# Kernel optimization log

Hardware: AMD Instinct MI355X
Metric: run time of the kernel (lower is better)

## Reference

```python
import jax, jax.numpy as jnp
import numpy as np

N = 100000
LS = (0, 1, 2)
MULS = (128, 64, 32)   # multiplicities of 0e,1o,2e in input1 / mid / out
MUL_Y = 64             # input2 = 64x0e (pure scalars)
DIM_X = sum(m * (2 * l + 1) for m, l in zip(MULS, LS))  # 480


def _split_irreps(x):
    # x: (N, 480) -> list of (N, mul, 2l+1) blocks
    parts, off = [], 0
    for m, l in zip(MULS, LS):
        d = m * (2 * l + 1)
        parts.append(x[:, off:off + d].reshape(-1, m, 2 * l + 1))
        off += d
    return parts


def setup_inputs() -> dict:
    key = jax.random.key(0)
    ks = jax.random.split(key, 8)
    inp = {
        "x": jax.random.normal(ks[0], (N, DIM_X), jnp.float32),
        "y": jax.random.normal(ks[1], (N, MUL_Y), jnp.float32),
    }
    for i, m in enumerate(MULS):
        # e3nn internal weights ~ N(0,1); path normalization applied in forward
        inp[f"W_tp{i}"] = jax.random.normal(ks[2 + i], (m, MUL_Y, m), jnp.float32)
        inp[f"W_lin{i}"] = jax.random.normal(ks[5 + i], (m, m), jnp.float32)
    return inp


def reference(x, y, W_tp0, W_tp1, W_tp2, W_lin0, W_lin1, W_lin2):
    W_tp = (W_tp0, W_tp1, W_tp2)
    W_lin = (W_lin0, W_lin1, W_lin2)
    xs = _split_irreps(x)
    outs = []
    for m, l, Wt, Wl, xl in zip(MULS, LS, W_tp, W_lin, xs):
        # e3nn 'uvw' path with scalar (0e) second input:
        #   CG(l,0,l)[m1,0,mo] = delta / sqrt(2l+1)
        #   path_weight = sqrt(ir_out.dim / (mul1*mul2)) = sqrt((2l+1)/(m*MUL_Y))
        # net coefficient = 1 / sqrt(m * MUL_Y)
        c_tp = float(1.0 / np.sqrt(m * MUL_Y))
        mid = c_tp * jnp.einsum('uvw,num,nv->nwm', Wt, xl, y)  # (N, m, 2l+1)
        # o3.Linear: single path per irrep, weight 1/sqrt(fan_in), fan_in = m
        c_lin = float(1.0 / np.sqrt(m))
        out = c_lin * jnp.einsum('uw,num->nwm', Wl, mid)       # (N, m, 2l+1)
        outs.append(out.reshape(-1, m * (2 * l + 1)))
    return jnp.concatenate(outs, axis=-1)  # (N, 480)
```

## Files before the change

### kernel.cpp

```cpp
#include <hip/hip_runtime.h>


typedef _Float16 f16x8 __attribute__((ext_vector_type(8)));
typedef _Float16 h2    __attribute__((ext_vector_type(2)));
typedef float    f32x4 __attribute__((ext_vector_type(4)));

__device__ __forceinline__ void gload_lds16(const void* g, void* l) {
    __builtin_amdgcn_global_load_lds(
        (const __attribute__((address_space(1))) unsigned*)g,
        (__attribute__((address_space(3))) unsigned*)l, 16, 0, 0);
}

template<int M, int NT>
__global__ void pack_b(const float* __restrict__ Wt, const float* __restrict__ Wl,
                       _Float16* __restrict__ Bp) {
    const int gid = blockIdx.x * 256 + threadIdx.x;
    const int total = M * 64 * M / 2;
    if (gid >= total) return;
    const int w_ = gid & (M - 1);
    const int uvp = gid / M;
    const float4* wtA = (const float4*)(Wt + (size_t)(2 * uvp) * M);
    const float4* wtB = (const float4*)(Wt + (size_t)(2 * uvp + 1) * M);
    float a0 = 0.f, a1 = 0.f;
    #pragma unroll 4
    for (int w = 0; w < M; w += 4) {
        float4 tA = wtA[w >> 2], tB = wtB[w >> 2];
        float l0 = Wl[(w + 0) * M + w_], l1 = Wl[(w + 1) * M + w_];
        float l2 = Wl[(w + 2) * M + w_], l3 = Wl[(w + 3) * M + w_];
        a0 += tA.x * l0 + tA.y * l1 + tA.z * l2 + tA.w * l3;
        a1 += tB.x * l0 + tB.y * l1 + tB.z * l2 + tB.w * l3;
    }
    #pragma unroll
    for (int t = 0; t < 2; ++t) {
        const int uv = 2 * uvp + t;
        const int u = uv >> 6, v = uv & 63;
        const int vh = v >> 5, vv = v & 31, quad = vv >> 3, j = vv & 7;
        const int kc = u * 2 + vh, nt = w_ >> 4, lane = quad * 16 + (w_ & 15);
        Bp[((size_t)(kc * NT + nt) * 64 + lane) * 8 + j] = (_Float16)(t ? a1 : a0);
    }
}

template<int M, int NCOMP, int XOFF, int NT, int KC, int MT>
__device__ __forceinline__ void tp_block(char* smem, int wg,
    const float* __restrict__ x, const float* __restrict__ y,
    const _Float16* __restrict__ Bp, float* __restrict__ out, int Rtot, float cscale)
{
    constexpr int WM = MT / 128;
    constexpr int WN = NT;
    constexpr int UC = KC / 2;
    constexpr int XU = 16;
    constexpr int KTOT = 2 * M;
    constexpr int NCHUNK = KTOT / KC;
    constexpr int CPS = XU / UC;
    constexpr int NSLAB = M / XU;
    constexpr int BCH = KC * NT * 1024;
    constexpr int XSL = MT * XU * 2;
    constexpr int NS_T = MT / NCOMP + 2;
    constexpr int XE = NS_T * XU * NCOMP;
    constexpr int XITER = (XE + 511) / 512;

    char* bb0 = smem;
    char* bb1 = smem + BCH;
    char* xb0 = smem + 2 * BCH;
    char* xb1 = smem + 2 * BCH + XSL;

    const int tid = threadIdx.x;
    const int lane = tid & 63;
    const int wv = tid >> 6;
    const int l15 = lane & 15;
    const int quad = lane >> 4;
    const int r0 = wg * MT;
    const int s0 = r0 / NCOMP;
    const int k0 = r0 - s0 * NCOMP;

    float xt[XITER];
    auto xld = [&](int slab) {
        const int ub = slab * XU;
        #pragma unroll
        for (int i = 0; i < XITER; ++i) {
            const int p = tid + i * 512;
            float v = 0.f;
            if (p < XE) {
                const int sl = p / (XU * NCOMP);
                const int fo = p - sl * (XU * NCOMP);
                const int ul = fo / NCOMP;
                const int k  = fo - ul * NCOMP;
                const int rl = sl * NCOMP + k - k0;
                if (rl >= 0 && rl < MT && (r0 + rl) < Rtot)
                    v = x[(size_t)(s0 + sl) * 480 + XOFF + (ub + ul) * NCOMP + k];
            }
            xt[i] = v;
        }
    };
    auto xwr = [&](char* xd) {
        #pragma unroll
        for (int i = 0; i < XITER; ++i) {
            const int p = tid + i * 512;
            if (p < XE) {
                const int sl = p / (XU * NCOMP);
                const int fo = p - sl * (XU * NCOMP);
                const int ul = fo / NCOMP;
                const int k  = fo - ul * NCOMP;
                const int rl = sl * NCOMP + k - k0;
                if (rl >= 0 && rl < MT)
                    *(_Float16*)(xd + (rl * XU + ul) * 2) = (_Float16)xt[i];
            }
        }
    };
    auto stageB = [&](int c, char* bd) {
        const char* gs = (const char*)Bp + (size_t)c * BCH + wv * 2048 + lane * 16;
        char* ld = bd + wv * 2048;
        gload_lds16(gs, ld);
        gload_lds16(gs + 1024, ld + 1024);
    };

    int rowf[WM];
    union YH { f16x8 v; h2 h[4]; };
    YH yh[2][WM];
    #pragma unroll
    for (int f = 0; f < WM; ++f) {
        rowf[f] = wv * (WM * 16) + f * 16 + l15;
        const int Rg = r0 + rowf[f];
        const int sf = (Rg < Rtot) ? (int)((unsigned)Rg / NCOMP) : 0;
        #pragma unroll
        for (int vh = 0; vh < 2; ++vh) {
            const float4* yp = (const float4*)(y + (size_t)sf * 64 + vh * 32 + quad * 8);
            const float4 a = yp[0], b = yp[1];
            union { f16x8 v; _Float16 e[8]; } t;
            t.e[0] = (_Float16)a.x; t.e[1] = (_Float16)a.y;
            t.e[2] = (_Float16)a.z; t.e[3] = (_Float16)a.w;
            t.e[4] = (_Float16)b.x; t.e[5] = (_Float16)b.y;
            t.e[6] = (_Float16)b.z; t.e[7] = (_Float16)b.w;
            yh[vh][f].v = t.v;
        }
    }

    f32x4 acc[WM][WN];
    #pragma unroll
    for (int f = 0; f < WM; ++f)
        #pragma unroll
        for (int g = 0; g < WN; ++g) acc[f][g] = f32x4{0.f, 0.f, 0.f, 0.f};

    xld(0);
    stageB(0, bb0);
    xwr(xb0);
    __syncthreads();

    int bcur = 0, xcur = 0;
    #pragma unroll 1
    for (int c = 0; c < NCHUNK; ++c) {
        if (c + 1 < NCHUNK) stageB(c + 1, bcur ? bb0 : bb1);
        const int cm = c & (CPS - 1);
        const int sl1 = c / CPS + 1;
        if (cm == 0 && sl1 < NSLAB) xld(sl1);

        const char* bs = bcur ? bb1 : bb0;
        const char* xs = xcur ? xb1 : xb0;
        const int uoff = cm * UC;
        unsigned xv0[WM], xv1[WM];
        #pragma unroll
        for (int f = 0; f < WM; ++f) {
            const char* xa = xs + (rowf[f] * XU + uoff) * 2;
            if constexpr (UC == 1)      xv0[f] = *(const unsigned short*)xa;
            else if constexpr (UC == 2) xv0[f] = *(const unsigned*)xa;
            else { const uint2 t = *(const uint2*)xa; xv0[f] = t.x; xv1[f] = t.y; }
        }
        #pragma unroll
        for (int kl = 0; kl < KC; ++kl) {
            const int vh = kl & 1, uo = kl >> 1;
            f16x8 bg[WN];
            #pragma unroll
            for (int g = 0; g < WN; ++g)
                bg[g] = *(const f16x8*)(bs + (kl * NT + g) * 1024 + lane * 16);
            f16x8 af[WM];
            #pragma unroll
            for (int f = 0; f < WM; ++f) {
                const unsigned d = (UC == 4 && (uo & 2)) ? xv1[f] : xv0[f];
                const unsigned hh = (uo & 1) ? (d >> 16) : (d & 0xffffu);
                union { unsigned u; h2 h; } xb2; xb2.u = hh | (hh << 16);
                union { f16x8 v; h2 h[4]; } a_;
                #pragma unroll
                for (int q = 0; q < 4; ++q) a_.h[q] = xb2.h * yh[vh][f].h[q];
                af[f] = a_.v;
            }
            #pragma unroll
            for (int f = 0; f < WM; ++f)
                #pragma unroll
                for (int g = 0; g < WN; ++g)
                    acc[f][g] = __builtin_amdgcn_mfma_f32_16x16x32_f16(af[f], bg[g], acc[f][g], 0, 0, 0);
        }
        if (cm == CPS - 1 && sl1 < NSLAB) xwr(xcur ? xb0 : xb1);
        __syncthreads();
        bcur ^= 1;
        if (cm == CPS - 1) xcur ^= 1;
    }

    #pragma unroll
    for (int f = 0; f < WM; ++f) {
        #pragma unroll
        for (int g = 0; g < WN; ++g) {
            const int col = g * 16 + l15;
            #pragma unroll
            for (int r = 0; r < 4; ++r) {
                const int R = r0 + wv * (WM * 16) + f * 16 + quad * 4 + r;
                if (R < Rtot) {
                    const int s = (int)((unsigned)R / NCOMP);
                    const int k = R - s * NCOMP;
                    out[(size_t)s * 480 + XOFF + col * NCOMP + k] = acc[f][g][r] * cscale;
                }
            }
        }
    }
}

__global__ __launch_bounds__(512, 2)
void tp_main(const float* __restrict__ x, const float* __restrict__ y,
             const _Float16* __restrict__ B0, const _Float16* __restrict__ B1,
             const _Float16* __restrict__ B2, float* __restrict__ out,
             int R0, int R1, int R2, int G0, int G1)
{
    __shared__ char smem[65536];
    const int b = blockIdx.x;
    if (b < G0)            tp_block<128, 1,   0, 8, 2, 384>(smem, b,           x, y, B0, out, R0, 1.f / 1024.f);
    else if (b < G0 + G1)  tp_block< 64, 3, 128, 4, 4, 512>(smem, b - G0,      x, y, B1, out, R1, 1.f / 512.f);
    else                   tp_block< 32, 5, 320, 2, 8, 512>(smem, b - G0 - G1, x, y, B2, out, R2, 1.f / 256.f);
}

extern "C" void kernel_launch(void* const* d_in, const int* in_sizes, int n_in,
                              void* d_out, int out_size, void* d_ws, size_t ws_size,
                              hipStream_t stream) {
    const float* x   = (const float*)d_in[0];
    const float* y   = (const float*)d_in[1];
    const float* Wt0 = (const float*)d_in[2];
    const float* Wl0 = (const float*)d_in[3];
    const float* Wt1 = (const float*)d_in[4];
    const float* Wl1 = (const float*)d_in[5];
    const float* Wt2 = (const float*)d_in[6];
    const float* Wl2 = (const float*)d_in[7];
    float* out = (float*)d_out;

    const int Ns = in_sizes[0] / 480;

    _Float16* B0 = (_Float16*)d_ws;
    _Float16* B1 = B0 + 8192 * 128;
    _Float16* B2 = B1 + 4096 * 64;

    pack_b<128, 8><<<(128 * 64 * 128 / 2 + 255) / 256, 256, 0, stream>>>(Wt0, Wl0, B0);
    pack_b< 64, 4><<<( 64 * 64 *  64 / 2 + 255) / 256, 256, 0, stream>>>(Wt1, Wl1, B1);
    pack_b< 32, 2><<<( 32 * 64 *  32 / 2 + 255) / 256, 256, 0, stream>>>(Wt2, Wl2, B2);

    const int R0 = Ns, R1 = Ns * 3, R2 = Ns * 5;
    const int G0 = (R0 + 383) / 384;
    const int G1 = (R1 + 511) / 512;
    const int G2 = (R2 + 511) / 512;
    tp_main<<<G0 + G1 + G2, 512, 0, stream>>>(x, y, B0, B1, B2, out, R0, R1, R2, G0, G1);
}
```

Before: 682.1 us.

## Use 4x2 wave tiling and store x as pre-duplicated half2 in padded LDS

Waves are rearranged from an 8x1 split along rows to a 4x2 grid over rows and output columns. Each wave now reads half the B fragments from LDS but builds twice as many A fragments (x times y). The x slab in LDS is now stored as pre-duplicated half2 words with a padded stride of 20, so the inner loop does one vector load and no shift-and-mask to build the broadcast. In exchange, static LDS grows from 64 KiB to 112 KiB. That likely cuts residency from two workgroups per CU to one and weakens latency hiding.

```diff
diff --git a/kernel.cpp b/kernel.cpp
--- a/kernel.cpp
+++ b/kernel.cpp
@@ -45,16 +45,18 @@
     const float* __restrict__ x, const float* __restrict__ y,
     const _Float16* __restrict__ Bp, float* __restrict__ out, int Rtot, float cscale)
 {
-    constexpr int WM = MT / 128;
-    constexpr int WN = NT;
+    constexpr int WAVES_M = 4, WAVES_N = 2;
+    constexpr int WM = MT / (WAVES_M * 16);
+    constexpr int WN = NT / WAVES_N;
     constexpr int UC = KC / 2;
     constexpr int XU = 16;
+    constexpr int XS = 20;
     constexpr int KTOT = 2 * M;
     constexpr int NCHUNK = KTOT / KC;
     constexpr int CPS = XU / UC;
     constexpr int NSLAB = M / XU;
     constexpr int BCH = KC * NT * 1024;
-    constexpr int XSL = MT * XU * 2;
+    constexpr int XSL = MT * XS * 4;
     constexpr int NS_T = MT / NCOMP + 2;
     constexpr int XE = NS_T * XU * NCOMP;
     constexpr int XITER = (XE + 511) / 512;
@@ -67,6 +69,8 @@
     const int tid = threadIdx.x;
     const int lane = tid & 63;
     const int wv = tid >> 6;
+    const int wvn = wv & 1;
+    const int wvm = wv >> 1;
     const int l15 = lane & 15;
     const int quad = lane >> 4;
     const int r0 = wg * MT;
@@ -102,8 +106,11 @@
                 const int ul = fo / NCOMP;
                 const int k  = fo - ul * NCOMP;
                 const int rl = sl * NCOMP + k - k0;
-                if (rl >= 0 && rl < MT)
-                    *(_Float16*)(xd + (rl * XU + ul) * 2) = (_Float16)xt[i];
+                if (rl >= 0 && rl < MT) {
+                    union { _Float16 h; unsigned short u; } cv; cv.h = (_Float16)xt[i];
+                    const unsigned pp = (unsigned)cv.u | ((unsigned)cv.u << 16);
+                    *(unsigned*)(xd + (unsigned)((rl * XS + ul) << 2)) = pp;
+                }
             }
         }
     };
@@ -119,7 +126,7 @@
     YH yh[2][WM];
     #pragma unroll
     for (int f = 0; f < WM; ++f) {
-        rowf[f] = wv * (WM * 16) + f * 16 + l15;
+        rowf[f] = wvm * (WM * 16) + f * 16 + l15;
         const int Rg = r0 + rowf[f];
         const int sf = (Rg < Rtot) ? (int)((unsigned)Rg / NCOMP) : 0;
         #pragma unroll
@@ -157,13 +164,14 @@
         const char* bs = bcur ? bb1 : bb0;
         const char* xs = xcur ? xb1 : xb0;
         const int uoff = cm * UC;
-        unsigned xv0[WM], xv1[WM];
+
+        uint4 xv[WM];
         #pragma unroll
         for (int f = 0; f < WM; ++f) {
-            const char* xa = xs + (rowf[f] * XU + uoff) * 2;
-            if constexpr (UC == 1)      xv0[f] = *(const unsigned short*)xa;
-            else if constexpr (UC == 2) xv0[f] = *(const unsigned*)xa;
-            else { const uint2 t = *(const uint2*)xa; xv0[f] = t.x; xv1[f] = t.y; }
+            const char* xa = xs + (unsigned)((rowf[f] * XS + uoff) << 2);
+            if constexpr (UC == 1)      { xv[f].x = *(const unsigned*)xa; }
+            else if constexpr (UC == 2) { const uint2 t = *(const uint2*)xa; xv[f].x = t.x; xv[f].y = t.y; }
+            else                        { xv[f] = *(const uint4*)xa; }
         }
         #pragma unroll
         for (int kl = 0; kl < KC; ++kl) {
@@ -171,13 +179,13 @@
             f16x8 bg[WN];
             #pragma unroll
             for (int g = 0; g < WN; ++g)
-                bg[g] = *(const f16x8*)(bs + (kl * NT + g) * 1024 + lane * 16);
+                bg[g] = *(const f16x8*)(bs + (unsigned)((kl * NT + wvn * WN + g) << 10) + lane * 16);
             f16x8 af[WM];
             #pragma unroll
             for (int f = 0; f < WM; ++f) {
-                const unsigned d = (UC == 4 && (uo & 2)) ? xv1[f] : xv0[f];
-                const unsigned hh = (uo & 1) ? (d >> 16) : (d & 0xffffu);
-                union { unsigned u; h2 h; } xb2; xb2.u = hh | (hh << 16);
+                const unsigned px = (uo == 0) ? xv[f].x : (uo == 1) ? xv[f].y
+                                  : (uo == 2) ? xv[f].z : xv[f].w;
+                union { unsigned u; h2 h; } xb2; xb2.u = px;
                 union { f16x8 v; h2 h[4]; } a_;
                 #pragma unroll
                 for (int q = 0; q < 4; ++q) a_.h[q] = xb2.h * yh[vh][f].h[q];
@@ -199,10 +207,10 @@
     for (int f = 0; f < WM; ++f) {
         #pragma unroll
         for (int g = 0; g < WN; ++g) {
-            const int col = g * 16 + l15;
+            const int col = (wvn * WN + g) * 16 + l15;
             #pragma unroll
             for (int r = 0; r < 4; ++r) {
-                const int R = r0 + wv * (WM * 16) + f * 16 + quad * 4 + r;
+                const int R = r0 + wvm * (WM * 16) + f * 16 + quad * 4 + r;
                 if (R < Rtot) {
                     const int s = (int)((unsigned)R / NCOMP);
                     const int k = R - s * NCOMP;
@@ -219,7 +227,7 @@
              const _Float16* __restrict__ B2, float* __restrict__ out,
              int R0, int R1, int R2, int G0, int G1)
 {
-    __shared__ char smem[65536];
+    __shared__ char smem[114688];
     const int b = blockIdx.x;
     if (b < G0)            tp_block<128, 1,   0, 8, 2, 384>(smem, b,           x, y, B0, out, R0, 1.f / 1024.f);
     else if (b < G0 + G1)  tp_block< 64, 3, 128, 4, 4, 512>(smem, b - G0,      x, y, B1, out, R1, 1.f / 512.f);
```

Measured after the change: 740.0 us. 8.5% more time.
